# Optimization experiments

Hardware: AMD Instinct MI355X
Metric: run time of the kernel (lower is better)

The kernel has to match this reference:

```python
import jax, jax.numpy as jnp
import numpy as np

DIM = 1024
NUM_HEADS = 16
HEAD_DIM = DIM // NUM_HEADS
N_PREFIX = 5
SCALE = HEAD_DIM ** -0.5


def _rotate_half(x):
    h = x.shape[-1] // 2
    return jnp.concatenate([-x[..., h:], x[..., :h]], axis=-1)


def _apply_rope(x, cos, sin):
    return x * cos + _rotate_half(x) * sin


def setup_inputs() -> dict:
    key = jax.random.key(0)
    ks = jax.random.split(key, 12)
    B, S = 8, N_PREFIX + 1024
    x = jax.random.normal(ks[0], (B, S, DIM), dtype=jnp.float32)
    rope_cos = jax.random.uniform(ks[1], (1024, HEAD_DIM), dtype=jnp.float32)
    rope_sin = jax.random.uniform(ks[2], (1024, HEAD_DIM), dtype=jnp.float32)
    sd = DIM ** -0.5
    Wq = jax.random.normal(ks[3], (DIM, DIM), dtype=jnp.float32) * sd
    bq = jnp.zeros((DIM,), dtype=jnp.float32)
    Wk = jax.random.normal(ks[4], (DIM, DIM), dtype=jnp.float32) * sd
    Wv = jax.random.normal(ks[5], (DIM, DIM), dtype=jnp.float32) * sd
    bv = jnp.zeros((DIM,), dtype=jnp.float32)
    Wo = jax.random.normal(ks[6], (DIM, DIM), dtype=jnp.float32) * sd
    bo = jnp.zeros((DIM,), dtype=jnp.float32)
    return {"x": x, "rope_cos": rope_cos, "rope_sin": rope_sin,
            "Wq": Wq, "bq": bq, "Wk": Wk, "Wv": Wv, "bv": bv,
            "Wo": Wo, "bo": bo}


def reference(x, rope_cos, rope_sin, Wq, bq, Wk, Wv, bv, Wo, bo):
    B, S, D = x.shape
    # projections: Q and V have bias, K has no bias
    q = (x @ Wq + bq).reshape(B, S, NUM_HEADS, HEAD_DIM).transpose(0, 2, 1, 3)
    k = (x @ Wk).reshape(B, S, NUM_HEADS, HEAD_DIM).transpose(0, 2, 1, 3)
    v = (x @ Wv + bv).reshape(B, S, NUM_HEADS, HEAD_DIM).transpose(0, 2, 1, 3)
    # 2D RoPE on patch tokens only (prefix tokens untouched)
    cos = rope_cos[None, None]  # [1,1,P,hd]
    sin = rope_sin[None, None]
    q = jnp.concatenate([q[:, :, :N_PREFIX], _apply_rope(q[:, :, N_PREFIX:], cos, sin)], axis=2)
    k = jnp.concatenate([k[:, :, :N_PREFIX], _apply_rope(k[:, :, N_PREFIX:], cos, sin)], axis=2)
    q = q * SCALE
    attn = jax.nn.softmax(jnp.einsum('bhqd,bhkd->bhqk', q, k), axis=-1)
    out = jnp.einsum('bhqk,bhkd->bhqd', attn, v)
    out = out.transpose(0, 2, 1, 3).reshape(B, S, D)
    return out @ Wo + bo
```

## Files before the change

### kernel.cpp

```cpp
#include <hip/hip_runtime.h>

typedef unsigned short u16;
typedef __bf16 bf16x8 __attribute__((ext_vector_type(8)));
typedef unsigned short u16x8 __attribute__((ext_vector_type(8)));
typedef float f32x4 __attribute__((ext_vector_type(4)));

#define M_ROWS 8232
#define SEQ 1029
#define NPREF 5
#define DIMN 1024
#define NH 16
#define HD 64

#define BAR_LGKM asm volatile("s_waitcnt lgkmcnt(0)\ns_barrier" ::: "memory")

__device__ __forceinline__ u16 f2bf(float f) {
  unsigned u = __float_as_uint(f);
  u += 0x7fffu + ((u >> 16) & 1u);
  return (u16)(u >> 16);
}

__device__ __forceinline__ unsigned pk2bf(float lo, float hi) {
  unsigned ul = __float_as_uint(lo);
  unsigned uh = __float_as_uint(hi);
  ul += 0x7fffu + ((ul >> 16) & 1u);
  uh += 0x7fffu + ((uh >> 16) & 1u);
  return __builtin_amdgcn_perm(uh, ul, 0x07060302u);
}

__global__ __launch_bounds__(256) void k_pack_x(const float* __restrict__ x, u16* __restrict__ Xp) {
  int cb = blockIdx.x;
  int rb = blockIdx.y;
  __shared__ u16 Tl[64 * 264];
  int t = threadIdx.x;
#pragma unroll
  for (int p = 0; p < 16; ++p) {
    int idx = p * 256 + t;
    int row = idx >> 6;
    int c4 = idx & 63;
    int grow = rb * 64 + row; if (grow >= M_ROWS) grow = M_ROWS - 1;
    float4 v = *reinterpret_cast<const float4*>(x + (size_t)grow * DIMN + cb * 256 + c4 * 4);
    ushort4 o;
    o.x = f2bf(v.x); o.y = f2bf(v.y); o.z = f2bf(v.z); o.w = f2bf(v.w);
    *reinterpret_cast<ushort4*>(&Tl[row * 264 + c4 * 4]) = o;
  }
  __syncthreads();
  int wv = t >> 6, lane = t & 63;
  int mt = rb >> 1, g = rb & 1;
#pragma unroll
  for (int li = 0; li < 8; ++li) {
    int ll = wv * 8 + li;
    int i = ll >> 3;
    int kkl = ll & 7;
    int row = i * 16 + (lane & 15);
    int col = kkl * 32 + (lane >> 4) * 8;
    uint4 d = *reinterpret_cast<const uint4*>(&Tl[row * 264 + col]);
    size_t line = ((size_t)(mt * 2 + g) * 4 + i) * 32 + (cb * 8 + kkl);
    *reinterpret_cast<uint4*>(Xp + line * 512 + lane * 8) = d;
  }
}

__global__ __launch_bounds__(256) void k_wt(const float* __restrict__ W0, const float* __restrict__ W1,
                                            const float* __restrict__ W2, const float* __restrict__ W3,
                                            u16* __restrict__ P0, u16* __restrict__ P1,
                                            u16* __restrict__ P2, u16* __restrict__ P3) {
  const float* W; u16* P;
  switch (blockIdx.z) {
    case 0: W = W0; P = P0; break;
    case 1: W = W1; P = P1; break;
    case 2: W = W2; P = P2; break;
    default: W = W3; P = P3; break;
  }
  __shared__ float tile[64 * 68];
  int t = threadIdx.x;
  int kb = blockIdx.x, nb = blockIdx.y;
#pragma unroll
  for (int p = 0; p < 16; ++p) {
    int idx = p * 256 + t;
    int row = idx >> 6, col = idx & 63;
    tile[row * 68 + col] = W[(size_t)(kb * 64 + row) * DIMN + nb * 64 + col];
  }
  __syncthreads();
  int wv = t >> 6, lane = t & 63;
#pragma unroll
  for (int li = 0; li < 2; ++li) {
    int ll = wv * 2 + li;
    int jg = ll >> 1, kkl = ll & 1;
    int n = jg * 16 + (lane & 15);
    int kc = kkl * 32 + (lane >> 4) * 8;
    u16 buf[8];
#pragma unroll
    for (int dk = 0; dk < 8; ++dk) buf[dk] = f2bf(tile[(kc + dk) * 68 + n]);
    size_t line = (size_t)(nb * 4 + jg) * 32 + kb * 2 + kkl;
    *reinterpret_cast<uint4*>(P + line * 512 + lane * 8) = *reinterpret_cast<const uint4*>(buf);
  }
}

#define MM16(AF, BF) do { \
  _Pragma("unroll") for (int i_ = 0; i_ < 4; ++i_) \
  _Pragma("unroll") for (int j_ = 0; j_ < 4; ++j_) \
    acc[i_][j_] = __builtin_amdgcn_mfma_f32_16x16x32_bf16(AF[i_], BF[j_], acc[i_][j_], 0, 0, 0); \
} while (0)

#define LDFRAG(AA, BB, KK) do { \
  _Pragma("unroll") for (int i_ = 0; i_ < 4; ++i_) { \
    AA[i_] = *reinterpret_cast<const bf16x8*>(abase + (size_t)i_ * 16384 + (size_t)(KK) * 512); \
    BB[i_] = *reinterpret_cast<const bf16x8*>(bbase + (size_t)i_ * 16384 + (size_t)(KK) * 512); \
  } } while (0)

__global__ __launch_bounds__(256) void k_qkv(
    const u16* __restrict__ Xp,
    const u16* __restrict__ Pq, const u16* __restrict__ Pk, const u16* __restrict__ Pv,
    const float* __restrict__ bq, const float* __restrict__ bv,
    const float* __restrict__ rc, const float* __restrict__ rs,
    u16* __restrict__ Qg, u16* __restrict__ Kg, u16* __restrict__ Vg)
{
  int bid = blockIdx.x;
  int xcd = bid & 7;
  int s = bid >> 3;
  int nt = s & 7;
  int s2 = s >> 3;
  int mode = s2 / 9;
  int mtq = s2 - mode * 9;
  int mt = mtq * 8 + xcd;
  if (mt >= 65) return;
  const u16* Wp = (mode == 0) ? Pq : (mode == 1) ? Pk : Pv;
  u16* dst = (mode == 0) ? Qg : (mode == 1) ? Kg : Vg;
  int m0 = mt * 128, n0 = nt * 128;

  int t = threadIdx.x, lane = t & 63, wv = t >> 6;
  int fr = lane & 15, quad = lane >> 4;
  int ga = wv >> 1, gb = wv & 1;
  int wm = ga * 64, wn = gb * 64;

  const u16* abase = Xp + ((size_t)(mt * 2 + ga) * 4 * 32) * 512 + lane * 8;
  const u16* bbase = Wp + ((size_t)(nt * 2 + gb) * 4 * 32) * 512 + lane * 8;

  f32x4 zero4 = {0.f, 0.f, 0.f, 0.f};
  f32x4 acc[4][4];
#pragma unroll
  for (int i = 0; i < 4; ++i)
#pragma unroll
    for (int j = 0; j < 4; ++j) acc[i][j] = zero4;

  bf16x8 a0[4], b0[4], a1[4], b1[4];
  LDFRAG(a0, b0, 0);
  for (int kk = 0; kk < 32; kk += 2) {
    if (kk + 1 < 32) LDFRAG(a1, b1, kk + 1);
    MM16(a0, b0);
    if (kk + 2 < 32) LDFRAG(a0, b0, kk + 2);
    MM16(a1, b1);
  }

  int h = (n0 + wn) >> 6;
#pragma unroll
  for (int i = 0; i < 4; ++i) {
    int rowbase = m0 + wm + i * 16 + quad * 4;
#pragma unroll
    for (int r = 0; r < 4; ++r) {
      int row = rowbase + r;
      if (row >= M_ROWS) continue;
      int b = row / SEQ;
      int sI = row - b * SEQ;
#pragma unroll
      for (int j = 0; j < 4; ++j) {
        int d = j * 16 + fr;
        float v = acc[i][j][r];
        float outv;
        if (mode == 2) {
          outv = v + bv[n0 + wn + d];
        } else {
          float vb = v;
          int jp = j ^ 2;
          float pv = acc[i][jp][r];
          if (mode == 0) {
            vb += bq[n0 + wn + d];
            pv += bq[n0 + wn + (jp * 16 + fr)];
          }
          if (sI >= NPREF) {
            int p = sI - NPREF;
            float c = rc[p * HD + d];
            float sn = rs[p * HD + d];
            float rot = (d < 32) ? -pv : pv;
            outv = vb * c + rot * sn;
          } else {
            outv = vb;
          }
          if (mode == 0) outv *= 0.125f;
        }
        dst[((size_t)(b * NH + h) * SEQ + sI) * HD + d] = f2bf(outv);
      }
    }
  }
}

__global__ __launch_bounds__(256) void k_attn(
    const u16* __restrict__ Qg, const u16* __restrict__ Kg, const u16* __restrict__ Vg,
    u16* __restrict__ AOp)
{
  int bh = blockIdx.x;
  int mtb = blockIdx.y;
  int q0 = mtb * 128;
  int b = bh >> 4, h = bh & 15;
  const size_t base = (size_t)bh * SEQ * HD;

  __shared__ u16 KV[128 * 72];
  __shared__ u16 Ps[4][32 * 72];
  u16* Ks = KV;
  u16* Vt = KV + 64 * 72;

  int t = threadIdx.x, lane = t & 63, wv = t >> 6;
  int fr = lane & 15, quad = lane >> 4;

  int ki = t >> 2;
  int kc0 = (t & 3) * 16;
  int vs0 = (t & 31) * 2;
  int vdo = (t >> 5) * 8;

  bf16x8 qf[2][2];
#pragma unroll
  for (int qt = 0; qt < 2; ++qt) {
#pragma unroll
    for (int st = 0; st < 2; ++st) {
      int row = q0 + wv * 32 + qt * 16 + fr;
      if (row >= SEQ) row = SEQ - 1;
      qf[qt][st] = *reinterpret_cast<const bf16x8*>(Qg + base + (size_t)row * HD + st * 32 + quad * 8);
    }
  }

  u16x8 one16 = {0x3F80, 0x3F80, 0x3F80, 0x3F80, 0x3F80, 0x3F80, 0x3F80, 0x3F80};
  bf16x8 vone = __builtin_bit_cast(bf16x8, one16);

  f32x4 zero4 = {0.f, 0.f, 0.f, 0.f};
  f32x4 o[2][5];
#pragma unroll
  for (int qt = 0; qt < 2; ++qt)
#pragma unroll
    for (int di = 0; di < 5; ++di) o[qt][di] = zero4;

  uint4 krA0, krA1, vrA0, vrA1;
  {
    int kr = ki; if (kr >= SEQ) kr = SEQ - 1;
    const u16* ksrc = Kg + base + (size_t)kr * HD;
    krA0 = *reinterpret_cast<const uint4*>(ksrc + kc0);
    krA1 = *reinterpret_cast<const uint4*>(ksrc + kc0 + 8);
    int r0 = vs0; if (r0 >= SEQ) r0 = SEQ - 1;
    int r1 = vs0 + 1; if (r1 >= SEQ) r1 = SEQ - 1;
    vrA0 = *reinterpret_cast<const uint4*>(Vg + base + (size_t)r0 * HD + vdo);
    vrA1 = *reinterpret_cast<const uint4*>(Vg + base + (size_t)r1 * HD + vdo);
  }

  for (int kt = 0; kt < 17; ++kt) {
    int k0 = kt * 64;
    BAR_LGKM;
    *reinterpret_cast<uint4*>(&Ks[ki * 72 + kc0]) = krA0;
    *reinterpret_cast<uint4*>(&Ks[ki * 72 + kc0 + 8]) = krA1;
    {
      u16 v0[8], v1[8];
      *reinterpret_cast<uint4*>(v0) = vrA0;
      *reinterpret_cast<uint4*>(v1) = vrA1;
#pragma unroll
      for (int j = 0; j < 8; ++j) {
        unsigned pk = (unsigned)v0[j] | ((unsigned)v1[j] << 16);
        *reinterpret_cast<unsigned*>(&Vt[(vdo + j) * 72 + vs0]) = pk;
      }
    }
    if (kt < 16) {
      int kn = k0 + 64;
      int kr = kn + ki; if (kr >= SEQ) kr = SEQ - 1;
      const u16* ksrc = Kg + base + (size_t)kr * HD;
      krA0 = *reinterpret_cast<const uint4*>(ksrc + kc0);
      krA1 = *reinterpret_cast<const uint4*>(ksrc + kc0 + 8);
      int r0 = kn + vs0; if (r0 >= SEQ) r0 = SEQ - 1;
      int r1 = kn + vs0 + 1; if (r1 >= SEQ) r1 = SEQ - 1;
      vrA0 = *reinterpret_cast<const uint4*>(Vg + base + (size_t)r0 * HD + vdo);
      vrA1 = *reinterpret_cast<const uint4*>(Vg + base + (size_t)r1 * HD + vdo);
    }
    BAR_LGKM;

    f32x4 sc[4][2];
#pragma unroll
    for (int mi = 0; mi < 4; ++mi)
#pragma unroll
      for (int qt = 0; qt < 2; ++qt) sc[mi][qt] = zero4;
#pragma unroll
    for (int st = 0; st < 2; ++st) {
#pragma unroll
      for (int mi = 0; mi < 4; ++mi) {
        bf16x8 kf = *reinterpret_cast<const bf16x8*>(&Ks[(mi * 16 + fr) * 72 + st * 32 + quad * 8]);
#pragma unroll
        for (int qt = 0; qt < 2; ++qt)
          sc[mi][qt] = __builtin_amdgcn_mfma_f32_16x16x32_bf16(kf, qf[qt][st], sc[mi][qt], 0, 0, 0);
      }
    }

    bool last = (kt == 16);
#pragma unroll
    for (int qt = 0; qt < 2; ++qt) {
#pragma unroll
      for (int mi = 0; mi < 4; ++mi) {
        float p0, p1, p2, p3;
        {
          float s0v = sc[mi][qt][0], s1v = sc[mi][qt][1], s2v = sc[mi][qt][2], s3v = sc[mi][qt][3];
          if (last) {
            int kc = mi * 16 + quad * 4;
            if (kc + 0 >= NPREF) s0v = -1e30f;
            if (kc + 1 >= NPREF) s1v = -1e30f;
            if (kc + 2 >= NPREF) s2v = -1e30f;
            if (kc + 3 >= NPREF) s3v = -1e30f;
          }
          p0 = __expf(s0v - 16.0f);
          p1 = __expf(s1v - 16.0f);
          p2 = __expf(s2v - 16.0f);
          p3 = __expf(s3v - 16.0f);
        }
        unsigned d0 = pk2bf(p0, p1);
        unsigned d1 = pk2bf(p2, p3);
        uint2 w; w.x = d0; w.y = d1;
        *reinterpret_cast<uint2*>(&Ps[wv][(qt * 16 + fr) * 72 + mi * 16 + quad * 4]) = w;
      }
    }

#pragma unroll
    for (int st = 0; st < 2; ++st) {
      bf16x8 pf[2];
#pragma unroll
      for (int qt = 0; qt < 2; ++qt)
        pf[qt] = *reinterpret_cast<const bf16x8*>(&Ps[wv][(qt * 16 + fr) * 72 + st * 32 + quad * 8]);
#pragma unroll
      for (int di = 0; di < 4; ++di) {
        bf16x8 vf = *reinterpret_cast<const bf16x8*>(&Vt[(di * 16 + fr) * 72 + st * 32 + quad * 8]);
#pragma unroll
        for (int qt = 0; qt < 2; ++qt)
          o[qt][di] = __builtin_amdgcn_mfma_f32_16x16x32_bf16(pf[qt], vf, o[qt][di], 0, 0, 0);
      }
#pragma unroll
      for (int qt = 0; qt < 2; ++qt)
        o[qt][4] = __builtin_amdgcn_mfma_f32_16x16x32_bf16(pf[qt], vone, o[qt][4], 0, 0, 0);
    }
  }

  __syncthreads();
#pragma unroll
  for (int qt = 0; qt < 2; ++qt) {
#pragma unroll
    for (int r = 0; r < 4; ++r) {
      int rowl = wv * 32 + qt * 16 + quad * 4 + r;
      bool valid = (q0 + rowl) < SEQ;
      float inv = valid ? (1.f / o[qt][4][r]) : 0.f;
#pragma unroll
      for (int di = 0; di < 4; ++di)
        KV[rowl * 72 + di * 16 + fr] = f2bf(o[qt][di][r] * inv);
    }
  }
  __syncthreads();
#pragma unroll
  for (int li = 0; li < 4; ++li) {
    int ll = wv * 4 + li;
    int g = ll >> 3, i = (ll >> 1) & 3, kkl = ll & 1;
    int rowl = g * 64 + i * 16 + (lane & 15);
    int col = kkl * 32 + (lane >> 4) * 8;
    uint4 d = *reinterpret_cast<const uint4*>(&KV[rowl * 72 + col]);
    size_t line = ((size_t)((b * 9 + mtb) * 2 + g) * 4 + i) * 32 + (h * 2 + kkl);
    *reinterpret_cast<uint4*>(AOp + line * 512 + lane * 8) = d;
  }
}

__global__ __launch_bounds__(256) void k_out(
    const u16* __restrict__ AOp, const u16* __restrict__ Po,
    const float* __restrict__ bo, float* __restrict__ Out)
{
  int bid = blockIdx.x;
  int xcd = bid & 7;
  int s = bid >> 3;
  int nt = s & 7;
  int mtq = s >> 3;
  int mid = mtq * 8 + xcd;
  int b = mid / 9, mtb = mid - b * 9;
  int n0 = nt * 128;

  int t = threadIdx.x, lane = t & 63, wv = t >> 6;
  int fr = lane & 15, quad = lane >> 4;
  int ga = wv >> 1, gb = wv & 1;
  int wm = ga * 64, wn = gb * 64;

  const u16* abase = AOp + ((size_t)(mid * 2 + ga) * 4 * 32) * 512 + lane * 8;
  const u16* bbase = Po + ((size_t)(nt * 2 + gb) * 4 * 32) * 512 + lane * 8;

  f32x4 zero4 = {0.f, 0.f, 0.f, 0.f};
  f32x4 acc[4][4];
#pragma unroll
  for (int i = 0; i < 4; ++i)
#pragma unroll
    for (int j = 0; j < 4; ++j) acc[i][j] = zero4;

  bf16x8 a0[4], b0[4], a1[4], b1[4];
  LDFRAG(a0, b0, 0);
  for (int kk = 0; kk < 32; kk += 2) {
    if (kk + 1 < 32) LDFRAG(a1, b1, kk + 1);
    MM16(a0, b0);
    if (kk + 2 < 32) LDFRAG(a0, b0, kk + 2);
    MM16(a1, b1);
  }

#pragma unroll
  for (int i = 0; i < 4; ++i) {
    int rowbase = mtb * 128 + wm + i * 16 + quad * 4;
#pragma unroll
    for (int r = 0; r < 4; ++r) {
      int rowl = rowbase + r;
      if (rowl >= SEQ) continue;
      size_t row = (size_t)b * SEQ + rowl;
#pragma unroll
      for (int j = 0; j < 4; ++j) {
        int col = n0 + wn + j * 16 + fr;
        Out[row * DIMN + col] = acc[i][j][r] + bo[col];
      }
    }
  }
}

extern "C" void kernel_launch(void* const* d_in, const int* in_sizes, int n_in,
                              void* d_out, int out_size, void* d_ws, size_t ws_size,
                              hipStream_t stream)
{
  const float* x  = (const float*)d_in[0];
  const float* rc = (const float*)d_in[1];
  const float* rs = (const float*)d_in[2];
  const float* Wq = (const float*)d_in[3];
  const float* bq = (const float*)d_in[4];
  const float* Wk = (const float*)d_in[5];
  const float* Wv = (const float*)d_in[6];
  const float* bv = (const float*)d_in[7];
  const float* Wo = (const float*)d_in[8];
  const float* bo = (const float*)d_in[9];
  float* Out = (float*)d_out;

  u16* p = (u16*)d_ws;
  u16* Xp = p; p += (size_t)16640 * 512;
  u16* Pq = p; p += (size_t)2048 * 512;
  u16* Pk = p; p += (size_t)2048 * 512;
  u16* Pv = p; p += (size_t)2048 * 512;
  u16* Po = p; p += (size_t)2048 * 512;
  u16* Qg = p; p += (size_t)M_ROWS * DIMN;
  u16* Kg = p; p += (size_t)M_ROWS * DIMN;
  u16* Vg = p; p += (size_t)M_ROWS * DIMN;
  u16* AOp = Xp;

  dim3 gx(4, 130);
  k_pack_x<<<gx, 256, 0, stream>>>(x, Xp);
  dim3 gt(16, 16, 4);
  k_wt<<<gt, 256, 0, stream>>>(Wq, Wk, Wv, Wo, Pq, Pk, Pv, Po);
  k_qkv<<<1728, 256, 0, stream>>>(Xp, Pq, Pk, Pv, bq, bv, rc, rs, Qg, Kg, Vg);
  dim3 g2(128, 9);
  k_attn<<<g2, 256, 0, stream>>>(Qg, Kg, Vg, AOp);
  k_out<<<576, 256, 0, stream>>>(AOp, Po, bo, Out);
}
```

Measured before the change: 336.5 us.

## Stage GEMM operand fragments through LDS with direct global-to-LDS loads

In the QKV and output projection GEMMs, each wave used to load its A and B fragments straight from global memory into registers, so every fragment was fetched by two waves. Now each k-step has the block's four waves cooperatively copy the 16 fragment lines into shared memory with global_load_lds, synchronize, and read their fragments back from LDS. This halves redundant global and L2 traffic. In exchange the LDS buffer is single, there are two block barriers per k-step, and the register double-buffered prefetch is gone, so load latency is no longer hidden behind MFMA work.

```diff
diff --git a/kernel.cpp b/kernel.cpp
--- a/kernel.cpp
+++ b/kernel.cpp
@@ -13,6 +13,13 @@
 #define HD 64
 
 #define BAR_LGKM asm volatile("s_waitcnt lgkmcnt(0)\ns_barrier" ::: "memory")
+
+typedef __attribute__((address_space(1))) const unsigned char as1_u8;
+typedef __attribute__((address_space(3))) unsigned char as3_u8;
+
+__device__ __forceinline__ void gload_lds16(const u16* g, u16* l) {
+  __builtin_amdgcn_global_load_lds((as1_u8*)g, (as3_u8*)l, 16, 0, 0);
+}
 
 __device__ __forceinline__ u16 f2bf(float f) {
   unsigned u = __float_as_uint(f);
@@ -101,12 +108,6 @@
   _Pragma("unroll") for (int j_ = 0; j_ < 4; ++j_) \
     acc[i_][j_] = __builtin_amdgcn_mfma_f32_16x16x32_bf16(AF[i_], BF[j_], acc[i_][j_], 0, 0, 0); \
 } while (0)
-
-#define LDFRAG(AA, BB, KK) do { \
-  _Pragma("unroll") for (int i_ = 0; i_ < 4; ++i_) { \
-    AA[i_] = *reinterpret_cast<const bf16x8*>(abase + (size_t)i_ * 16384 + (size_t)(KK) * 512); \
-    BB[i_] = *reinterpret_cast<const bf16x8*>(bbase + (size_t)i_ * 16384 + (size_t)(KK) * 512); \
-  } } while (0)
 
 __global__ __launch_bounds__(256) void k_qkv(
     const u16* __restrict__ Xp,
@@ -133,8 +134,34 @@
   int ga = wv >> 1, gb = wv & 1;
   int wm = ga * 64, wn = gb * 64;
 
-  const u16* abase = Xp + ((size_t)(mt * 2 + ga) * 4 * 32) * 512 + lane * 8;
-  const u16* bbase = Wp + ((size_t)(nt * 2 + gb) * 4 * 32) * 512 + lane * 8;
+  __shared__ u16 S[16][512];
+
+  const u16* gsrc[4];
+  u16* ldst[4];
+#pragma unroll
+  for (int q = 0; q < 4; ++q) {
+    int ls = wv * 4 + q;
+    const u16* base;
+    int lineIdx;
+    if (ls < 8) {
+      int g = ls >> 2, i = ls & 3;
+      base = Xp; lineIdx = ((mt * 2 + g) * 4 + i) * 32;
+    } else {
+      int l2 = ls - 8;
+      int g = l2 >> 2, j = l2 & 3;
+      base = Wp; lineIdx = ((nt * 2 + g) * 4 + j) * 32;
+    }
+    gsrc[q] = base + (size_t)lineIdx * 512 + lane * 8;
+    ldst[q] = &S[ls][0];
+  }
+
+  const u16* ards[4];
+  const u16* brds[4];
+#pragma unroll
+  for (int i = 0; i < 4; ++i) {
+    ards[i] = &S[ga * 4 + i][lane * 8];
+    brds[i] = &S[8 + gb * 4 + i][lane * 8];
+  }
 
   f32x4 zero4 = {0.f, 0.f, 0.f, 0.f};
   f32x4 acc[4][4];
@@ -143,13 +170,19 @@
 #pragma unroll
     for (int j = 0; j < 4; ++j) acc[i][j] = zero4;
 
-  bf16x8 a0[4], b0[4], a1[4], b1[4];
-  LDFRAG(a0, b0, 0);
-  for (int kk = 0; kk < 32; kk += 2) {
-    if (kk + 1 < 32) LDFRAG(a1, b1, kk + 1);
-    MM16(a0, b0);
-    if (kk + 2 < 32) LDFRAG(a0, b0, kk + 2);
-    MM16(a1, b1);
+  for (int kk = 0; kk < 32; ++kk) {
+#pragma unroll
+    for (int q = 0; q < 4; ++q)
+      gload_lds16(gsrc[q] + (size_t)kk * 512, ldst[q]);
+    __syncthreads();
+    bf16x8 a[4], b[4];
+#pragma unroll
+    for (int i = 0; i < 4; ++i) {
+      a[i] = *reinterpret_cast<const bf16x8*>(ards[i]);
+      b[i] = *reinterpret_cast<const bf16x8*>(brds[i]);
+    }
+    MM16(a, b);
+    __syncthreads();
   }
 
   int h = (n0 + wn) >> 6;
@@ -384,8 +417,34 @@
   int ga = wv >> 1, gb = wv & 1;
   int wm = ga * 64, wn = gb * 64;
 
-  const u16* abase = AOp + ((size_t)(mid * 2 + ga) * 4 * 32) * 512 + lane * 8;
-  const u16* bbase = Po + ((size_t)(nt * 2 + gb) * 4 * 32) * 512 + lane * 8;
+  __shared__ u16 S[16][512];
+
+  const u16* gsrc[4];
+  u16* ldst[4];
+#pragma unroll
+  for (int q = 0; q < 4; ++q) {
+    int ls = wv * 4 + q;
+    const u16* base;
+    int lineIdx;
+    if (ls < 8) {
+      int g = ls >> 2, i = ls & 3;
+      base = AOp; lineIdx = ((mid * 2 + g) * 4 + i) * 32;
+    } else {
+      int l2 = ls - 8;
+      int g = l2 >> 2, j = l2 & 3;
+      base = Po; lineIdx = ((nt * 2 + g) * 4 + j) * 32;
+    }
+    gsrc[q] = base + (size_t)lineIdx * 512 + lane * 8;
+    ldst[q] = &S[ls][0];
+  }
+
+  const u16* ards[4];
+  const u16* brds[4];
+#pragma unroll
+  for (int i = 0; i < 4; ++i) {
+    ards[i] = &S[ga * 4 + i][lane * 8];
+    brds[i] = &S[8 + gb * 4 + i][lane * 8];
+  }
 
   f32x4 zero4 = {0.f, 0.f, 0.f, 0.f};
   f32x4 acc[4][4];
@@ -394,13 +453,19 @@
 #pragma unroll
     for (int j = 0; j < 4; ++j) acc[i][j] = zero4;
 
-  bf16x8 a0[4], b0[4], a1[4], b1[4];
-  LDFRAG(a0, b0, 0);
-  for (int kk = 0; kk < 32; kk += 2) {
-    if (kk + 1 < 32) LDFRAG(a1, b1, kk + 1);
-    MM16(a0, b0);
-    if (kk + 2 < 32) LDFRAG(a0, b0, kk + 2);
-    MM16(a1, b1);
+  for (int kk = 0; kk < 32; ++kk) {
+#pragma unroll
+    for (int q = 0; q < 4; ++q)
+      gload_lds16(gsrc[q] + (size_t)kk * 512, ldst[q]);
+    __syncthreads();
+    bf16x8 a[4], b2[4];
+#pragma unroll
+    for (int i = 0; i < 4; ++i) {
+      a[i] = *reinterpret_cast<const bf16x8*>(ards[i]);
+      b2[i] = *reinterpret_cast<const bf16x8*>(brds[i]);
+    }
+    MM16(a, b2);
+    __syncthreads();
   }
 
 #pragma unroll
```

Result: no change. 336.6 us (+0.0%).

## Stage QKV GEMM tiles through LDS with async triple-buffered loads and larger tiles

Applied to the files above, without the earlier changes.

The QKV projection GEMM now uses 256x128 block tiles. Operands are streamed into a three-stage LDS ring with global_load_lds, using vmcnt waits and barriers in place of direct per-wave global fragment loads. Each wave now computes a 64x128 slice that reuses the shared B tile, and the grid shrinks accordingly. The change also adds s_setprio around the MFMA sections in both the QKV and attention kernels. It trades higher register and LDS use and a per-step barrier for less redundant global traffic and overlapped loads.

```diff
diff --git a/kernel.cpp b/kernel.cpp
--- a/kernel.cpp
+++ b/kernel.cpp
@@ -13,6 +13,13 @@
 #define HD 64
 
 #define BAR_LGKM asm volatile("s_waitcnt lgkmcnt(0)\ns_barrier" ::: "memory")
+
+typedef __attribute__((address_space(1))) const unsigned char as1_u8;
+typedef __attribute__((address_space(3))) unsigned char as3_u8;
+
+__device__ __forceinline__ void gload_lds16(const u16* g, u16* l) {
+  __builtin_amdgcn_global_load_lds((as1_u8*)g, (as3_u8*)l, 16, 0, 0);
+}
 
 __device__ __forceinline__ u16 f2bf(float f) {
   unsigned u = __float_as_uint(f);
@@ -108,7 +115,7 @@
     BB[i_] = *reinterpret_cast<const bf16x8*>(bbase + (size_t)i_ * 16384 + (size_t)(KK) * 512); \
   } } while (0)
 
-__global__ __launch_bounds__(256) void k_qkv(
+__global__ __launch_bounds__(256, 2) void k_qkv(
     const u16* __restrict__ Xp,
     const u16* __restrict__ Pq, const u16* __restrict__ Pk, const u16* __restrict__ Pv,
     const float* __restrict__ bq, const float* __restrict__ bv,
@@ -120,42 +127,78 @@
   int s = bid >> 3;
   int nt = s & 7;
   int s2 = s >> 3;
-  int mode = s2 / 9;
-  int mtq = s2 - mode * 9;
-  int mt = mtq * 8 + xcd;
-  if (mt >= 65) return;
+  int mode = s2 / 5;
+  int mtq = s2 - mode * 5;
+  int mt2 = mtq * 8 + xcd;
+  if (mt2 >= 33) return;
   const u16* Wp = (mode == 0) ? Pq : (mode == 1) ? Pk : Pv;
   u16* dst = (mode == 0) ? Qg : (mode == 1) ? Kg : Vg;
-  int m0 = mt * 128, n0 = nt * 128;
+  int m0 = mt2 * 256, n0 = nt * 128;
 
   int t = threadIdx.x, lane = t & 63, wv = t >> 6;
   int fr = lane & 15, quad = lane >> 4;
-  int ga = wv >> 1, gb = wv & 1;
-  int wm = ga * 64, wn = gb * 64;
-
-  const u16* abase = Xp + ((size_t)(mt * 2 + ga) * 4 * 32) * 512 + lane * 8;
-  const u16* bbase = Wp + ((size_t)(nt * 2 + gb) * 4 * 32) * 512 + lane * 8;
+
+  __shared__ u16 S[3 * 24 * 512];
+  u16* Sb = S;
+
+  const u16* gsrc[6];
+#pragma unroll
+  for (int q = 0; q < 6; ++q) {
+    int ls = wv * 6 + q;
+    const u16* base;
+    int lineIdx;
+    if (ls < 16) { base = Xp; lineIdx = (mt2 * 16 + ls) * 32; }
+    else         { base = Wp; lineIdx = (nt * 8 + (ls - 16)) * 32; }
+    gsrc[q] = base + (size_t)lineIdx * 512 + lane * 8;
+  }
+
+#define QSTAGE(bufI, tt) do { \
+  _Pragma("unroll") for (int q_ = 0; q_ < 6; ++q_) \
+    gload_lds16(gsrc[q_] + (size_t)(tt) * 512, Sb + (bufI) * 12288 + (wv * 6 + q_) * 512); \
+} while (0)
 
   f32x4 zero4 = {0.f, 0.f, 0.f, 0.f};
-  f32x4 acc[4][4];
+  f32x4 acc[4][8];
 #pragma unroll
   for (int i = 0; i < 4; ++i)
 #pragma unroll
-    for (int j = 0; j < 4; ++j) acc[i][j] = zero4;
-
-  bf16x8 a0[4], b0[4], a1[4], b1[4];
-  LDFRAG(a0, b0, 0);
-  for (int kk = 0; kk < 32; kk += 2) {
-    if (kk + 1 < 32) LDFRAG(a1, b1, kk + 1);
-    MM16(a0, b0);
-    if (kk + 2 < 32) LDFRAG(a0, b0, kk + 2);
-    MM16(a1, b1);
-  }
-
-  int h = (n0 + wn) >> 6;
+    for (int j = 0; j < 8; ++j) acc[i][j] = zero4;
+
+  QSTAGE(0, 0);
+  QSTAGE(1, 1);
+#pragma unroll
+  for (int kk = 0; kk < 32; ++kk) {
+    if (kk < 31) {
+      asm volatile("s_waitcnt vmcnt(6)" ::: "memory");
+    } else {
+      asm volatile("s_waitcnt vmcnt(0)" ::: "memory");
+    }
+    __builtin_amdgcn_s_barrier();
+    asm volatile("" ::: "memory");
+    if (kk + 2 < 32) QSTAGE((kk + 2) % 3, kk + 2);
+    const u16* rd_ = Sb + (kk % 3) * 12288;
+    bf16x8 a_[4], b_[8];
+#pragma unroll
+    for (int i = 0; i < 4; ++i)
+      a_[i] = *reinterpret_cast<const bf16x8*>(rd_ + (wv * 4 + i) * 512 + lane * 8);
+#pragma unroll
+    for (int j = 0; j < 8; ++j)
+      b_[j] = *reinterpret_cast<const bf16x8*>(rd_ + (16 + j) * 512 + lane * 8);
+    __builtin_amdgcn_s_setprio(1);
+#pragma unroll
+    for (int i = 0; i < 4; ++i)
+#pragma unroll
+      for (int j = 0; j < 8; ++j)
+        acc[i][j] = __builtin_amdgcn_mfma_f32_16x16x32_bf16(a_[i], b_[j], acc[i][j], 0, 0, 0);
+    __builtin_amdgcn_s_setprio(0);
+    asm volatile("" ::: "memory");
+  }
+  asm volatile("s_waitcnt vmcnt(0)" ::: "memory");
+#undef QSTAGE
+
 #pragma unroll
   for (int i = 0; i < 4; ++i) {
-    int rowbase = m0 + wm + i * 16 + quad * 4;
+    int rowbase = m0 + wv * 64 + i * 16 + quad * 4;
 #pragma unroll
     for (int r = 0; r < 4; ++r) {
       int row = rowbase + r;
@@ -163,32 +206,33 @@
       int b = row / SEQ;
       int sI = row - b * SEQ;
 #pragma unroll
-      for (int j = 0; j < 4; ++j) {
-        int d = j * 16 + fr;
+      for (int j = 0; j < 8; ++j) {
+        int h = nt * 2 + (j >> 2);
+        int dh = (j & 3) * 16 + fr;
         float v = acc[i][j][r];
         float outv;
         if (mode == 2) {
-          outv = v + bv[n0 + wn + d];
+          outv = v + bv[n0 + j * 16 + fr];
         } else {
           float vb = v;
           int jp = j ^ 2;
           float pv = acc[i][jp][r];
           if (mode == 0) {
-            vb += bq[n0 + wn + d];
-            pv += bq[n0 + wn + (jp * 16 + fr)];
+            vb += bq[n0 + j * 16 + fr];
+            pv += bq[n0 + jp * 16 + fr];
           }
           if (sI >= NPREF) {
             int p = sI - NPREF;
-            float c = rc[p * HD + d];
-            float sn = rs[p * HD + d];
-            float rot = (d < 32) ? -pv : pv;
+            float c = rc[p * HD + dh];
+            float sn = rs[p * HD + dh];
+            float rot = (dh < 32) ? -pv : pv;
             outv = vb * c + rot * sn;
           } else {
             outv = vb;
           }
           if (mode == 0) outv *= 0.125f;
         }
-        dst[((size_t)(b * NH + h) * SEQ + sI) * HD + d] = f2bf(outv);
+        dst[((size_t)(b * NH + h) * SEQ + sI) * HD + dh] = f2bf(outv);
       }
     }
   }
@@ -283,6 +327,7 @@
     for (int mi = 0; mi < 4; ++mi)
 #pragma unroll
       for (int qt = 0; qt < 2; ++qt) sc[mi][qt] = zero4;
+    __builtin_amdgcn_s_setprio(1);
 #pragma unroll
     for (int st = 0; st < 2; ++st) {
 #pragma unroll
@@ -293,6 +338,7 @@
           sc[mi][qt] = __builtin_amdgcn_mfma_f32_16x16x32_bf16(kf, qf[qt][st], sc[mi][qt], 0, 0, 0);
       }
     }
+    __builtin_amdgcn_s_setprio(0);
 
     bool last = (kt == 16);
 #pragma unroll
@@ -327,6 +373,7 @@
 #pragma unroll
       for (int qt = 0; qt < 2; ++qt)
         pf[qt] = *reinterpret_cast<const bf16x8*>(&Ps[wv][(qt * 16 + fr) * 72 + st * 32 + quad * 8]);
+      __builtin_amdgcn_s_setprio(1);
 #pragma unroll
       for (int di = 0; di < 4; ++di) {
         bf16x8 vf = *reinterpret_cast<const bf16x8*>(&Vt[(di * 16 + fr) * 72 + st * 32 + quad * 8]);
@@ -337,6 +384,7 @@
 #pragma unroll
       for (int qt = 0; qt < 2; ++qt)
         o[qt][4] = __builtin_amdgcn_mfma_f32_16x16x32_bf16(pf[qt], vone, o[qt][4], 0, 0, 0);
+      __builtin_amdgcn_s_setprio(0);
     }
   }
 
@@ -451,7 +499,7 @@
   k_pack_x<<<gx, 256, 0, stream>>>(x, Xp);
   dim3 gt(16, 16, 4);
   k_wt<<<gt, 256, 0, stream>>>(Wq, Wk, Wv, Wo, Pq, Pk, Pv, Po);
-  k_qkv<<<1728, 256, 0, stream>>>(Xp, Pq, Pk, Pv, bq, bv, rc, rs, Qg, Kg, Vg);
+  k_qkv<<<960, 256, 0, stream>>>(Xp, Pq, Pk, Pv, bq, bv, rc, rs, Qg, Kg, Vg);
   dim3 g2(128, 9);
   k_attn<<<g2, 256, 0, stream>>>(Qg, Kg, Vg, AOp);
   k_out<<<576, 256, 0, stream>>>(AOp, Po, bo, Out);
```

Measured after the change: 330.7 us. About the same (-1.7%).
